# Optimization experiments

Hardware: AMD Instinct MI355X
Metric: run time of the kernel (lower is better)

## Reference

```python
import jax, jax.numpy as jnp
import numpy as np

B, T, D = 4, 2048, 2048
H = 16
HD = D // H  # head_dim = 128


def setup_inputs() -> dict:
    key = jax.random.key(0)
    ks = jax.random.split(key, 10)
    s = 0.02
    return {
        "x": jax.random.normal(ks[0], (B, T, D), dtype=jnp.float32),
        "Wq": jax.random.normal(ks[1], (D, D), dtype=jnp.float32) * s,
        "bq": jnp.zeros((D,), dtype=jnp.float32),
        "Wk": jax.random.normal(ks[2], (D, D), dtype=jnp.float32) * s,
        "bk": jnp.zeros((D,), dtype=jnp.float32),
        "Wv": jax.random.normal(ks[3], (D, D), dtype=jnp.float32) * s,
        "bv": jnp.zeros((D,), dtype=jnp.float32),
        "Wo": jax.random.normal(ks[4], (D, D), dtype=jnp.float32) * s,
        "bo": jnp.zeros((D,), dtype=jnp.float32),
    }


def reference(x, Wq, bq, Wk, bk, Wv, bv, Wo, bo):
    b, t, _ = x.shape
    # projections (nn.Linear: x @ W.T + b); split heads -> (b, h, t, hd)
    def split_heads(y):
        return y.reshape(b, t, H, HD).transpose(0, 2, 1, 3)

    q = split_heads(x @ Wq.T + bq)
    k = split_heads(x @ Wk.T + bk)
    v = split_heads(x @ Wv.T + bv)

    scale = 1.0 / jnp.sqrt(jnp.float32(HD))
    scores = jnp.einsum("bhqd,bhkd->bhqk", q, k) * scale  # (b,h,t,t)
    causal = jnp.triu(jnp.ones((t, t), dtype=bool), k=1)
    scores = jnp.where(causal, -jnp.inf, scores)
    attn = jax.nn.softmax(scores, axis=-1)
    # dropout p=0.0 -> identity
    ctx = jnp.einsum("bhqk,bhkd->bhqd", attn, v)  # (b,h,t,hd)
    ctx = ctx.transpose(0, 2, 1, 3).reshape(b, t, D)
    return ctx @ Wo.T + bo
```

## Files before the change

### kernel.cpp

```cpp
#include <hip/hip_runtime.h>
#include <hip/hip_bf16.h>

typedef __attribute__((ext_vector_type(8))) __bf16 bf16x8;
typedef __attribute__((ext_vector_type(4))) __bf16 bf16x4;
typedef __attribute__((ext_vector_type(4))) short s16x4;
typedef __attribute__((ext_vector_type(4))) float f32x4;
typedef unsigned int u32;

#define LOG2E 1.4426950408889634f

__device__ __forceinline__ void gload_lds16(const void* g, void* l) {
  __builtin_amdgcn_global_load_lds(
      (const __attribute__((address_space(1))) u32*)g,
      (__attribute__((address_space(3))) u32*)l, 16, 0, 0);
}

__global__ __launch_bounds__(256)
void cvt_f32_bf16(const float* __restrict__ src, __hip_bfloat16* __restrict__ dst, int n4) {
  int i = blockIdx.x * blockDim.x + threadIdx.x;
  if (i < n4) {
    float4 v = ((const float4*)src)[i];
    union { unsigned long long u; __hip_bfloat16 h[4]; } o;
    o.h[0] = __float2bfloat16(v.x);
    o.h[1] = __float2bfloat16(v.y);
    o.h[2] = __float2bfloat16(v.z);
    o.h[3] = __float2bfloat16(v.w);
    ((unsigned long long*)dst)[i] = o.u;
  }
}

__global__ __launch_bounds__(256)
void cvt_all(const float* __restrict__ x,
             const float* __restrict__ w0, const float* __restrict__ w1,
             const float* __restrict__ w2, const float* __restrict__ w3,
             __hip_bfloat16* __restrict__ xb,
             __hip_bfloat16* __restrict__ b0, __hip_bfloat16* __restrict__ b1,
             __hip_bfloat16* __restrict__ b2, __hip_bfloat16* __restrict__ b3,
             int n4x, int n4wlog)
{
  int i = blockIdx.x * blockDim.x + threadIdx.x;
  const float* src; __hip_bfloat16* dst; int off;
  if (i < n4x) { src = x; dst = xb; off = i; }
  else {
    int j = i - n4x;
    int which = j >> n4wlog;
    off = j & ((1 << n4wlog) - 1);
    src = which == 0 ? w0 : which == 1 ? w1 : which == 2 ? w2 : w3;
    dst = which == 0 ? b0 : which == 1 ? b1 : which == 2 ? b2 : b3;
  }
  float4 v = ((const float4*)src)[off];
  union { unsigned long long u; __hip_bfloat16 h[4]; } o;
  o.h[0] = __float2bfloat16(v.x);
  o.h[1] = __float2bfloat16(v.y);
  o.h[2] = __float2bfloat16(v.z);
  o.h[3] = __float2bfloat16(v.w);
  ((unsigned long long*)dst)[off] = o.u;
}

#define VMW(N) asm volatile("s_waitcnt vmcnt(" #N ")" ::: "memory")

#define GPHASE(P, MH, NH, RDA, RDB, ISSUE, WAITC, LGHINT)                      \
  {                                                                            \
    if (RDA) {                                                                 \
      _Pragma("unroll")                                                        \
      for (int i = 0; i < 4; ++i) {                                            \
        const char* pa = Ab + (((MH) * 128 + wr * 64 + i * 16 + l15) << 7);    \
        afr[i][0] = *(const bf16x8*)(pa + ph0);                                \
        afr[i][1] = *(const bf16x8*)(pa + ph1);                                \
      }                                                                        \
    }                                                                          \
    if (RDB) {                                                                 \
      _Pragma("unroll")                                                        \
      for (int j = 0; j < 2; ++j) {                                            \
        const char* pb = Bb + (((NH) * 128 + wc * 32 + j * 16 + l15) << 7);    \
        bfr[j][0] = *(const bf16x8*)(pb + ph0);                                \
        bfr[j][1] = *(const bf16x8*)(pb + ph1);                                \
      }                                                                        \
    }                                                                          \
    ISSUE;                                                                     \
    WAITC;                                                                     \
    LGHINT;                                                                    \
    __builtin_amdgcn_s_barrier();                                              \
    asm volatile("s_waitcnt lgkmcnt(0)" ::: "memory");                         \
    __builtin_amdgcn_sched_barrier(0);                                         \
    __builtin_amdgcn_s_setprio(1);                                             \
    _Pragma("unroll")                                                          \
    for (int ks = 0; ks < 2; ++ks)                                             \
      _Pragma("unroll")                                                        \
      for (int i = 0; i < 4; ++i)                                              \
        _Pragma("unroll")                                                      \
        for (int j = 0; j < 2; ++j)                                            \
          acc[P][i][j] = __builtin_amdgcn_mfma_f32_16x16x32_bf16(              \
              afr[i][ks], bfr[j][ks], acc[P][i][j], 0, 0, 0);                  \
    __builtin_amdgcn_s_setprio(0);                                             \
    __builtin_amdgcn_s_barrier();                                              \
  }

#define GEMM_KLOOP()                                                           \
  auto issueA = [&](int t2, int mh) {                                          \
    if (t2 < NT) {                                                             \
      const __hip_bfloat16* g = Ag + (size_t)(mh * 128) * K + (t2 << 6);       \
      char* l = (char*)SH[t2 & 1] + mh * 16384 + (tid << 4);                   \
      gload_lds16(g, l);                                                       \
      gload_lds16(g + (size_t)64 * K, l + 8192);                               \
    }                                                                          \
  };                                                                           \
  auto issueB = [&](int t2, int nh) {                                          \
    if (t2 < NT) {                                                             \
      const __hip_bfloat16* g = Wg + (size_t)(nh * 128) * K + (t2 << 6);       \
      char* l = (char*)SH[t2 & 1] + 32768 + nh * 16384 + (tid << 4);           \
      gload_lds16(g, l);                                                       \
      gload_lds16(g + (size_t)64 * K, l + 8192);                               \
    }                                                                          \
  };                                                                           \
  issueA(0, 0); issueB(0, 0); issueB(0, 1); issueA(0, 1);                      \
  VMW(4);                                                                      \
  __builtin_amdgcn_s_barrier();                                                \
  for (int t = 0; t < NT; ++t) {                                               \
    const char* Ab = (const char*)SH[t & 1];                                   \
    const char* Bb = Ab + 32768;                                               \
    const bool more = (t + 1 < NT);                                            \
    GPHASE(0, 0, 0, true, true, issueA(t + 1, 0),                              \
           if (more) { VMW(4); } else { VMW(2); },                             \
           asm volatile("s_waitcnt lgkmcnt(8)" ::: "memory"));                 \
    GPHASE(1, 0, 1, false, true, issueB(t + 1, 0),                             \
           if (more) { VMW(4); } else { VMW(0); }, );                          \
    GPHASE(2, 1, 1, true, false, issueB(t + 1, 1), , );                        \
    GPHASE(3, 1, 0, false, true, issueA(t + 1, 1),                             \
           if (more) { VMW(4); }, );                                           \
  }

__global__ __launch_bounds__(512, 2)
void gemm_qkv(const __hip_bfloat16* __restrict__ A,
              const __hip_bfloat16* __restrict__ W3,
              const float* __restrict__ bq, const float* __restrict__ bk,
              const float* __restrict__ bv,
              __hip_bfloat16* __restrict__ Qb, __hip_bfloat16* __restrict__ Kb,
              __hip_bfloat16* __restrict__ Vtb,
              int M, int K, float qscale)
{
  __shared__ __align__(16) __hip_bfloat16 SH[2][32768];

  const int tid = threadIdx.x;
  const int lane = tid & 63;
  const int w = tid >> 6;
  const int wr = w >> 2, wc = w & 3;
  const int quad = lane >> 4, l15 = lane & 15;

  const int nb = 24;
  const int swz = (blockIdx.x & 7) * ((int)gridDim.x >> 3) + ((int)blockIdx.x >> 3);
  const int m0 = (swz / nb) << 8;
  const int n0 = (swz % nb) << 8;

  const int NT = K >> 6;

  const int r0 = tid >> 3;
  const int kb = ((tid & 7) ^ (r0 & 7)) << 3;
  const __hip_bfloat16* Ag = A + (size_t)(m0 + r0) * K + kb;
  const __hip_bfloat16* Wg = W3 + (size_t)(n0 + r0) * K + kb;

  const int ph0 = (quad ^ (l15 & 7)) << 4;
  const int ph1 = ((4 + quad) ^ (l15 & 7)) << 4;

  f32x4 acc[4][4][2] = {};
  bf16x8 afr[4][2], bfr[2][2];

  GEMM_KLOOP();

  const int which = n0 >> 11;
  const int nl0 = n0 & 2047;
  const float* bias = which == 0 ? bq : which == 1 ? bk : bv;
  const float oscale = which == 0 ? qscale : 1.0f;
  __hip_bfloat16* Cq = which == 0 ? Qb : Kb;

#pragma unroll
  for (int p = 0; p < 4; ++p) {
    const int mh = (p >= 2) ? 1 : 0;
    const int nh = (p == 1 || p == 2) ? 1 : 0;
#pragma unroll
    for (int i = 0; i < 4; ++i) {
      int mbase = m0 + mh * 128 + wr * 64 + i * 16 + quad * 4;
#pragma unroll
      for (int j = 0; j < 2; ++j) {
        int nl = nl0 + nh * 128 + wc * 32 + j * 16 + l15;
        float bvv = bias[nl];
#pragma unroll
        for (int r = 0; r < 4; ++r) {
          int mm = mbase + r;
          float v = (acc[p][i][j][r] + bvv) * oscale;
          if (which != 2) {
            Cq[(size_t)mm * 2048 + nl] = __float2bfloat16(v);
          } else {
            int b = mm >> 11, tt = mm & 2047;
            Vtb[((size_t)(b * 2048 + nl)) * 2048 + tt] = __float2bfloat16(v);
          }
        }
      }
    }
  }
}

template<int MODE>
__global__ __launch_bounds__(512, 2)
void gemm256(const __hip_bfloat16* __restrict__ A,
             const __hip_bfloat16* __restrict__ W,
             const float* __restrict__ bias,
             __hip_bfloat16* __restrict__ C,
             float* __restrict__ Cf,
             int M, int N, int K, float oscale)
{
  __shared__ __align__(16) __hip_bfloat16 SH[2][32768];

  const int tid = threadIdx.x;
  const int lane = tid & 63;
  const int w = tid >> 6;
  const int wr = w >> 2, wc = w & 3;
  const int quad = lane >> 4, l15 = lane & 15;

  const int nb = N >> 8;
  const int swz = (blockIdx.x & 7) * ((int)gridDim.x >> 3) + ((int)blockIdx.x >> 3);
  const int m0 = (swz / nb) << 8;
  const int n0 = (swz % nb) << 8;

  const int NT = K >> 6;

  const int r0 = tid >> 3;
  const int kb = ((tid & 7) ^ (r0 & 7)) << 3;
  const __hip_bfloat16* Ag = A + (size_t)(m0 + r0) * K + kb;
  const __hip_bfloat16* Wg = W + (size_t)(n0 + r0) * K + kb;

  const int ph0 = (quad ^ (l15 & 7)) << 4;
  const int ph1 = ((4 + quad) ^ (l15 & 7)) << 4;

  f32x4 acc[4][4][2] = {};
  bf16x8 afr[4][2], bfr[2][2];

  GEMM_KLOOP();

#pragma unroll
  for (int p = 0; p < 4; ++p) {
    const int mh = (p >= 2) ? 1 : 0;
    const int nh = (p == 1 || p == 2) ? 1 : 0;
#pragma unroll
    for (int i = 0; i < 4; ++i) {
      int mbase = m0 + mh * 128 + wr * 64 + i * 16 + quad * 4;
#pragma unroll
      for (int j = 0; j < 2; ++j) {
        int n = n0 + nh * 128 + wc * 32 + j * 16 + l15;
        float bv = bias[n];
#pragma unroll
        for (int r = 0; r < 4; ++r) {
          int mm = mbase + r;
          float v = (acc[p][i][j][r] + bv) * oscale;
          if (MODE == 0) {
            C[(size_t)mm * N + n] = __float2bfloat16(v);
          } else if (MODE == 1) {
            int b = mm >> 11, tt = mm & 2047;
            C[((size_t)(b * 2048 + n)) * 2048 + tt] = __float2bfloat16(v);
          } else {
            Cf[(size_t)mm * N + n] = v;
          }
        }
      }
    }
  }
}

__global__ __launch_bounds__(256, 2)
void attn_fwd(const __hip_bfloat16* __restrict__ Q,
              const __hip_bfloat16* __restrict__ K,
              const __hip_bfloat16* __restrict__ Vt,
              __hip_bfloat16* __restrict__ ctx)
{
  __shared__ __align__(16) __hip_bfloat16 KVl[2][16384];

  const int tid = threadIdx.x;
  const int lane = tid & 63;
  const int w = tid >> 6;
  const int quad = lane >> 4, l15 = lane & 15;
  const int bid = blockIdx.x;
  const int qi = 15 - (bid >> 6);
  const int bh = bid & 63;
  const int b = bh >> 4, h = bh & 15;
  const int q0 = qi * 128;

  bf16x8 qf[2][4];
  for (int sub = 0; sub < 2; ++sub) {
    const __hip_bfloat16* qp =
        Q + ((size_t)(b * 2048 + q0 + sub * 64 + w * 16 + l15)) * 2048 + h * 128 + quad * 8;
    for (int ks = 0; ks < 4; ++ks) qf[sub][ks] = *(const bf16x8*)(qp + ks * 32);
  }

  int krow[4], kcol[4], vrow[4], vcol[4], soff[4];
  for (int p = 0; p < 4; ++p) {
    int off = (tid + p * 256) * 16;
    soff[p] = off;
    int r1 = off >> 8;
    int pc1 = (off >> 4) & 15;
    krow[p] = r1; kcol[p] = ((pc1 & 8) | ((pc1 & 7) ^ (r1 & 7))) * 8;
    int r2 = off >> 7;
    int pc2 = (off >> 4) & 7;
    vrow[p] = r2; vcol[p] = (pc2 ^ (r2 & 7)) * 8;
  }

  f32x4 o[2][8] = {};
  float lsum[2] = {0.f, 0.f};
  const int base0 = q0 + w * 16;
  const int base1 = q0 + 64 + w * 16;

  const int ktmax = (q0 + 127) >> 6;

  for (int p = 0; p < 4; ++p)
    gload_lds16(K + ((size_t)(b * 2048 + krow[p])) * 2048 + h * 128 + kcol[p],
                (char*)&KVl[0][0] + soff[p]);
  for (int p = 0; p < 4; ++p)
    gload_lds16(Vt + ((size_t)(b * 2048 + h * 128 + vrow[p])) * 2048 + vcol[p],
                (char*)&KVl[0][8192] + soff[p]);
  __syncthreads();

  for (int kt = 0; kt <= ktmax; ++kt) {
    const int cur = kt & 1;
    const int kbase = kt * 64;
    if (kt < ktmax) {
      const int nbase = kbase + 64;
      for (int p = 0; p < 4; ++p)
        gload_lds16(K + ((size_t)(b * 2048 + nbase + krow[p])) * 2048 + h * 128 + kcol[p],
                    (char*)&KVl[1 - cur][0] + soff[p]);
      for (int p = 0; p < 4; ++p)
        gload_lds16(Vt + ((size_t)(b * 2048 + h * 128 + vrow[p])) * 2048 + nbase + vcol[p],
                    (char*)&KVl[1 - cur][8192] + soff[p]);
    }

    const char* Kl = (const char*)&KVl[cur][0];
    const char* Vl = (const char*)&KVl[cur][8192];

    const bool act0 = kbase <= base0 + 15;
    const bool act1 = kbase <= base1 + 15;

    f32x4 s[2][4] = {};
#pragma unroll
    for (int ct = 0; ct < 4; ++ct) {
      int row = ct * 16 + l15;
#pragma unroll
      for (int ks = 0; ks < 4; ++ks) {
        int c = ks * 4 + quad;
        int ph = (c & 8) | ((c & 7) ^ (row & 7));
        bf16x8 kf = *(const bf16x8*)(Kl + row * 256 + ph * 16);
        if (act0) s[0][ct] = __builtin_amdgcn_mfma_f32_16x16x32_bf16(kf, qf[0][ks], s[0][ct], 0, 0, 0);
        if (act1) s[1][ct] = __builtin_amdgcn_mfma_f32_16x16x32_bf16(kf, qf[1][ks], s[1][ct], 0, 0, 0);
      }
    }

    union pu { bf16x4 h[2]; bf16x8 v; };
    pu pf8[2][2];
#pragma unroll
    for (int sub = 0; sub < 2; ++sub) {
      if (!(sub ? act1 : act0)) continue;
      const int bs = sub ? base1 : base0;
      const bool full = (kbase + 63 <= bs);
      float lsv = lsum[sub];
#pragma unroll
      for (int ct = 0; ct < 4; ++ct) {
        bf16x4 pb;
        if (full) {
#pragma unroll
          for (int r = 0; r < 4; ++r) {
            float e = exp2f(s[sub][ct][r]);
            lsv += e; pb[r] = (__bf16)e;
          }
        } else {
          int diff = (bs + l15) - (kbase + ct * 16 + quad * 4);
#pragma unroll
          for (int r = 0; r < 4; ++r) {
            float e = (r <= diff) ? exp2f(s[sub][ct][r]) : 0.f;
            lsv += e; pb[r] = (__bf16)e;
          }
        }
        pf8[sub][ct >> 1].h[ct & 1] = pb;
      }
      lsum[sub] = lsv;
    }

    const int h8 = (quad & 1) * 8;
    const int qh = quad >> 1;
#pragma unroll
    for (int dgrp = 0; dgrp < 8; ++dgrp) {
      int row = dgrp * 16 + l15;
      int rx = row & 7;
      const char* vrow_p = Vl + row * 128;
#pragma unroll
      for (int c = 0; c < 2; ++c) {
        int ch1 = 4 * c + qh;
        union { struct { s16x4 a, b; } s; bf16x8 v; } vu;
        vu.s.a = *(const s16x4*)(vrow_p + ((ch1 ^ rx) * 16) + h8);
        vu.s.b = *(const s16x4*)(vrow_p + (((ch1 + 2) ^ rx) * 16) + h8);
        if (act0) o[0][dgrp] = __builtin_amdgcn_mfma_f32_16x16x32_bf16(vu.v, pf8[0][c].v, o[0][dgrp], 0, 0, 0);
        if (act1) o[1][dgrp] = __builtin_amdgcn_mfma_f32_16x16x32_bf16(vu.v, pf8[1][c].v, o[1][dgrp], 0, 0, 0);
      }
    }
    __syncthreads();
  }

  for (int sub = 0; sub < 2; ++sub) {
    float ls = lsum[sub];
    ls += __shfl_xor(ls, 16, 64);
    ls += __shfl_xor(ls, 32, 64);
    lsum[sub] = 1.0f / ls;
  }

  for (int sub = 0; sub < 2; ++sub) {
    char* rb = (char*)&KVl[0][0] + (w * 2 + sub) * 4096;
    float inv = lsum[sub];
    for (int dgrp = 0; dgrp < 8; ++dgrp) {
      for (int rp = 0; rp < 2; ++rp) {
        __hip_bfloat16 lo = __float2bfloat16(o[sub][dgrp][rp * 2] * inv);
        __hip_bfloat16 hi = __float2bfloat16(o[sub][dgrp][rp * 2 + 1] * inv);
        u32 pk = (u32)*(unsigned short*)&lo | ((u32)*(unsigned short*)&hi << 16);
        int c = dgrp * 2 + (quad >> 1);
        int cp = c ^ (l15 & 7);
        *(u32*)(rb + l15 * 256 + cp * 16 + (quad & 1) * 8 + rp * 4) = pk;
      }
    }
    int q2 = lane & 15;
    int qq = q0 + sub * 64 + w * 16 + q2;
    __hip_bfloat16* cp = ctx + ((size_t)(b * 2048 + qq)) * 2048 + h * 128;
    for (int rr = 0; rr < 4; ++rr) {
      int cl = quad + rr * 4;
      int cph = cl ^ (q2 & 7);
      uint4 val = *(const uint4*)(rb + q2 * 256 + cph * 16);
      *(uint4*)(cp + cl * 8) = val;
    }
  }
}

extern "C" void kernel_launch(void* const* d_in, const int* in_sizes, int n_in,
                              void* d_out, int out_size, void* d_ws, size_t ws_size,
                              hipStream_t stream)
{
  (void)in_sizes; (void)n_in; (void)out_size;
  const float* x  = (const float*)d_in[0];
  const float* Wq = (const float*)d_in[1];
  const float* bq = (const float*)d_in[2];
  const float* Wk = (const float*)d_in[3];
  const float* bk = (const float*)d_in[4];
  const float* Wv = (const float*)d_in[5];
  const float* bv = (const float*)d_in[6];
  const float* Wo = (const float*)d_in[7];
  const float* bo = (const float*)d_in[8];
  float* out = (float*)d_out;

  const int M = 8192, D = 2048;
  const size_t MD = (size_t)M * D, DD = (size_t)D * D;
  const int n4x = (int)(MD / 4), n4w = (int)(DD / 4);
  dim3 cb(256), bb(256), ga(1024);
  dim3 gg((M / 256) * (D / 256)), gbb(512);
  dim3 gq((M / 256) * (3 * D / 256));
  const float qscale = 0.08838834764831845f * LOG2E;

  if (ws_size >= (4 * MD + 4 * DD) * 2) {
    __hip_bfloat16* xb  = (__hip_bfloat16*)d_ws;
    __hip_bfloat16* Wqb = xb  + MD;
    __hip_bfloat16* Wkb = Wqb + DD;
    __hip_bfloat16* Wvb = Wkb + DD;
    __hip_bfloat16* Wob = Wvb + DD;
    __hip_bfloat16* Qb  = Wob + DD;
    __hip_bfloat16* Kb  = Qb  + MD;
    __hip_bfloat16* Vtb = Kb  + MD;
    __hip_bfloat16* Cx  = xb;

    int tot4 = n4x + 4 * n4w;
    hipLaunchKernelGGL(cvt_all, dim3(tot4 / 256), cb, 0, stream,
                       x, Wq, Wk, Wv, Wo, xb, Wqb, Wkb, Wvb, Wob, n4x, 20);
    hipLaunchKernelGGL(gemm_qkv, gq, gbb, 0, stream,
                       xb, Wqb, bq, bk, bv, Qb, Kb, Vtb, M, D, qscale);
    hipLaunchKernelGGL(attn_fwd, ga, bb, 0, stream, Qb, Kb, Vtb, Cx);
    hipLaunchKernelGGL((gemm256<2>), gg, gbb, 0, stream, Cx, Wob, bo, (__hip_bfloat16*)nullptr, out, M, D, D, 1.0f);
  } else {
    __hip_bfloat16* xb  = (__hip_bfloat16*)d_ws;
    __hip_bfloat16* Wb  = xb  + MD;
    __hip_bfloat16* Qb  = Wb  + DD;
    __hip_bfloat16* Kb  = Qb  + MD;
    __hip_bfloat16* Vtb = Kb  + MD;
    __hip_bfloat16* Cx  = xb;

    dim3 cgx((n4x + 255) / 256), cgw((n4w + 255) / 256);
    hipLaunchKernelGGL(cvt_f32_bf16, cgx, cb, 0, stream, x, xb, n4x);
    hipLaunchKernelGGL(cvt_f32_bf16, cgw, cb, 0, stream, Wq, Wb, n4w);
    hipLaunchKernelGGL((gemm256<0>), gg, gbb, 0, stream, xb, Wb, bq, Qb, (float*)nullptr, M, D, D, qscale);
    hipLaunchKernelGGL(cvt_f32_bf16, cgw, cb, 0, stream, Wk, Wb, n4w);
    hipLaunchKernelGGL((gemm256<0>), gg, gbb, 0, stream, xb, Wb, bk, Kb, (float*)nullptr, M, D, D, 1.0f);
    hipLaunchKernelGGL(cvt_f32_bf16, cgw, cb, 0, stream, Wv, Wb, n4w);
    hipLaunchKernelGGL((gemm256<1>), gg, gbb, 0, stream, xb, Wb, bv, Vtb, (float*)nullptr, M, D, D, 1.0f);
    hipLaunchKernelGGL(attn_fwd, ga, bb, 0, stream, Qb, Kb, Vtb, Cx);
    hipLaunchKernelGGL(cvt_f32_bf16, cgw, cb, 0, stream, Wo, Wb, n4w);
    hipLaunchKernelGGL((gemm256<2>), gg, gbb, 0, stream, Cx, Wb, bo, (__hip_bfloat16*)nullptr, out, M, D, D, 1.0f);
  }
}
```

Measured before the change: 568.1 us.

## Deepen GEMM global-to-LDS prefetch and use XCD-aware tile mapping

The GEMM k-loop is restructured so that half-tiles for step t+2 are issued into LDS as soon as their quadrants of the current buffer have been read into registers. Two B-fragment register sets are kept so phases 3 and 4 reuse registers instead of rereading LDS, which keeps more loads in flight and removes one B reload per step. Block-to-tile mapping is replaced by an XCD-aware layout that gives each XCD a contiguous 4-row M band, aiming at better L2 reuse. The mapping hardcodes 32 M-tiles and a multiple of 8 N-tiles, and the added fragment registers raise register pressure.

```diff
diff --git a/kernel.cpp b/kernel.cpp
--- a/kernel.cpp
+++ b/kernel.cpp
@@ -59,44 +59,40 @@
 
 #define VMW(N) asm volatile("s_waitcnt vmcnt(" #N ")" ::: "memory")
 
-#define GPHASE(P, MH, NH, RDA, RDB, ISSUE, WAITC, LGHINT)                      \
-  {                                                                            \
-    if (RDA) {                                                                 \
+#define RD_A(MH)                                                               \
+  _Pragma("unroll")                                                            \
+  for (int i = 0; i < 4; ++i) {                                                \
+    const char* pa = Ab + (((MH) * 128 + wr * 64 + i * 16 + l15) << 7);        \
+    afr[i][0] = *(const bf16x8*)(pa + ph0);                                    \
+    afr[i][1] = *(const bf16x8*)(pa + ph1);                                    \
+  }
+
+#define RD_B(BF, NH)                                                           \
+  _Pragma("unroll")                                                            \
+  for (int j = 0; j < 2; ++j) {                                                \
+    const char* pb = Bb + (((NH) * 128 + wc * 32 + j * 16 + l15) << 7);        \
+    BF[j][0] = *(const bf16x8*)(pb + ph0);                                     \
+    BF[j][1] = *(const bf16x8*)(pb + ph1);                                     \
+  }
+
+#define BARRIER_DRAIN()                                                        \
+  __builtin_amdgcn_s_barrier();                                                \
+  asm volatile("s_waitcnt lgkmcnt(0)" ::: "memory");                           \
+  __builtin_amdgcn_sched_barrier(0)
+
+#define MFMA8(P, BF)                                                           \
+  __builtin_amdgcn_s_setprio(1);                                               \
+  _Pragma("unroll")                                                            \
+  for (int ks = 0; ks < 2; ++ks)                                               \
+    _Pragma("unroll")                                                          \
+    for (int i = 0; i < 4; ++i)                                                \
       _Pragma("unroll")                                                        \
-      for (int i = 0; i < 4; ++i) {                                            \
-        const char* pa = Ab + (((MH) * 128 + wr * 64 + i * 16 + l15) << 7);    \
-        afr[i][0] = *(const bf16x8*)(pa + ph0);                                \
-        afr[i][1] = *(const bf16x8*)(pa + ph1);                                \
-      }                                                                        \
-    }                                                                          \
-    if (RDB) {                                                                 \
-      _Pragma("unroll")                                                        \
-      for (int j = 0; j < 2; ++j) {                                            \
-        const char* pb = Bb + (((NH) * 128 + wc * 32 + j * 16 + l15) << 7);    \
-        bfr[j][0] = *(const bf16x8*)(pb + ph0);                                \
-        bfr[j][1] = *(const bf16x8*)(pb + ph1);                                \
-      }                                                                        \
-    }                                                                          \
-    ISSUE;                                                                     \
-    WAITC;                                                                     \
-    LGHINT;                                                                    \
-    __builtin_amdgcn_s_barrier();                                              \
-    asm volatile("s_waitcnt lgkmcnt(0)" ::: "memory");                         \
-    __builtin_amdgcn_sched_barrier(0);                                         \
-    __builtin_amdgcn_s_setprio(1);                                             \
-    _Pragma("unroll")                                                          \
-    for (int ks = 0; ks < 2; ++ks)                                             \
-      _Pragma("unroll")                                                        \
-      for (int i = 0; i < 4; ++i)                                              \
-        _Pragma("unroll")                                                      \
-        for (int j = 0; j < 2; ++j)                                            \
-          acc[P][i][j] = __builtin_amdgcn_mfma_f32_16x16x32_bf16(              \
-              afr[i][ks], bfr[j][ks], acc[P][i][j], 0, 0, 0);                  \
-    __builtin_amdgcn_s_setprio(0);                                             \
-    __builtin_amdgcn_s_barrier();                                              \
-  }
-
-#define GEMM_KLOOP()                                                           \
+      for (int j = 0; j < 2; ++j)                                              \
+        acc[P][i][j] = __builtin_amdgcn_mfma_f32_16x16x32_bf16(                \
+            afr[i][ks], BF[j][ks], acc[P][i][j], 0, 0, 0);                     \
+  __builtin_amdgcn_s_setprio(0)
+
+#define GEMM_S2_LOOP()                                                         \
   auto issueA = [&](int t2, int mh) {                                          \
     if (t2 < NT) {                                                             \
       const __hip_bfloat16* g = Ag + (size_t)(mh * 128) * K + (t2 << 6);       \
@@ -113,22 +109,46 @@
       gload_lds16(g + (size_t)64 * K, l + 8192);                               \
     }                                                                          \
   };                                                                           \
+   \
   issueA(0, 0); issueB(0, 0); issueB(0, 1); issueA(0, 1);                      \
-  VMW(4);                                                                      \
+  issueA(1, 0); issueB(1, 0);                                                  \
+  VMW(8);                                                                      \
   __builtin_amdgcn_s_barrier();                                                \
   for (int t = 0; t < NT; ++t) {                                               \
     const char* Ab = (const char*)SH[t & 1];                                   \
     const char* Bb = Ab + 32768;                                               \
-    const bool more = (t + 1 < NT);                                            \
-    GPHASE(0, 0, 0, true, true, issueA(t + 1, 0),                              \
-           if (more) { VMW(4); } else { VMW(2); },                             \
-           asm volatile("s_waitcnt lgkmcnt(8)" ::: "memory"));                 \
-    GPHASE(1, 0, 1, false, true, issueB(t + 1, 0),                             \
-           if (more) { VMW(4); } else { VMW(0); }, );                          \
-    GPHASE(2, 1, 1, true, false, issueB(t + 1, 1), , );                        \
-    GPHASE(3, 1, 0, false, true, issueA(t + 1, 1),                             \
-           if (more) { VMW(4); }, );                                           \
-  }
+                    \
+    issueB(t + 1, 1); issueA(t + 1, 1);                                        \
+    RD_B(b0fr, 0);                                                             \
+    RD_A(0);                                                                   \
+    if (t + 1 < NT) { VMW(8); } else { VMW(0); }                               \
+    BARRIER_DRAIN();                                                           \
+    MFMA8(0, b0fr);                                                            \
+    __builtin_amdgcn_s_barrier();                                              \
+                                                        \
+    RD_B(b1fr, 1);                                                             \
+    BARRIER_DRAIN();                                                           \
+    MFMA8(1, b1fr);                                                            \
+    __builtin_amdgcn_s_barrier();                                              \
+                                      \
+    issueA(t + 2, 0); issueB(t + 2, 0);                                        \
+    RD_A(1);                                                                   \
+    BARRIER_DRAIN();                                                           \
+    MFMA8(2, b1fr);                                                            \
+    __builtin_amdgcn_s_barrier();                                              \
+                                     \
+    if (t + 2 < NT) { VMW(8); } else if (t + 1 < NT) { VMW(4); } else { VMW(0); } \
+    BARRIER_DRAIN();                                                           \
+    MFMA8(3, b0fr);                                                            \
+    __builtin_amdgcn_s_barrier();                                              \
+  }
+
+#define XCD_MAP()                                                              \
+  const int xcd = blockIdx.x & 7;                                              \
+  const int idx = (int)blockIdx.x >> 3;                                        \
+  const int rr = idx >> 5, pos = idx & 31;                                     \
+  const int m0 = (xcd * 4 + (pos >> 3)) << 8;                                  \
+  const int n0 = (rr * 8 + (pos & 7)) << 8
 
 __global__ __launch_bounds__(512, 2)
 void gemm_qkv(const __hip_bfloat16* __restrict__ A,
@@ -147,10 +167,7 @@
   const int wr = w >> 2, wc = w & 3;
   const int quad = lane >> 4, l15 = lane & 15;
 
-  const int nb = 24;
-  const int swz = (blockIdx.x & 7) * ((int)gridDim.x >> 3) + ((int)blockIdx.x >> 3);
-  const int m0 = (swz / nb) << 8;
-  const int n0 = (swz % nb) << 8;
+  XCD_MAP();
 
   const int NT = K >> 6;
 
@@ -163,9 +180,9 @@
   const int ph1 = ((4 + quad) ^ (l15 & 7)) << 4;
 
   f32x4 acc[4][4][2] = {};
-  bf16x8 afr[4][2], bfr[2][2];
-
-  GEMM_KLOOP();
+  bf16x8 afr[4][2], b0fr[2][2], b1fr[2][2];
+
+  GEMM_S2_LOOP();
 
   const int which = n0 >> 11;
   const int nl0 = n0 & 2047;
@@ -217,10 +234,7 @@
   const int wr = w >> 2, wc = w & 3;
   const int quad = lane >> 4, l15 = lane & 15;
 
-  const int nb = N >> 8;
-  const int swz = (blockIdx.x & 7) * ((int)gridDim.x >> 3) + ((int)blockIdx.x >> 3);
-  const int m0 = (swz / nb) << 8;
-  const int n0 = (swz % nb) << 8;
+  XCD_MAP();
 
   const int NT = K >> 6;
 
@@ -233,9 +247,9 @@
   const int ph1 = ((4 + quad) ^ (l15 & 7)) << 4;
 
   f32x4 acc[4][4][2] = {};
-  bf16x8 afr[4][2], bfr[2][2];
-
-  GEMM_KLOOP();
+  bf16x8 afr[4][2], b0fr[2][2], b1fr[2][2];
+
+  GEMM_S2_LOOP();
 
 #pragma unroll
   for (int p = 0; p < 4; ++p) {
```

After: 541.6 us. 1.05x faster.
